# Kernel tuning notes

Measured on AMD Instinct MI355X. Metric: run time of the kernel, lower is better.

Reference implementation:

```python
import jax, jax.numpy as jnp
import numpy as np

N = 50000      # nodes
E = 800000     # edges (before self loops)
D_IN = 64      # input atom feature dim
HID = 128      # hidden_dim
HEADS = 4
C = HID // HEADS  # 32 per-head channels
ED = 12        # edge feature dim
L = 4          # num GAT layers
EPS = 1e-5


def setup_inputs() -> dict:
    key = jax.random.key(0)
    ks = jax.random.split(key, 10)
    s = 0.1
    return {
        "x": jax.random.normal(ks[0], (N, D_IN), jnp.float32),
        "edge_index": jax.random.randint(ks[1], (2, E), 0, N, dtype=jnp.int32),
        "edge_attr": jax.random.uniform(ks[2], (E, ED), jnp.float32),
        "Wp": jax.random.normal(ks[3], (D_IN, HID), jnp.float32) * s,
        "bp": jnp.zeros((HID,), jnp.float32),
        "W": jax.random.normal(ks[4], (L, HID, HID), jnp.float32) * s,
        "We": jax.random.normal(ks[5], (L, ED, HID), jnp.float32) * s,
        "att_src": jax.random.normal(ks[6], (L, HEADS, C), jnp.float32) * s,
        "att_dst": jax.random.normal(ks[7], (L, HEADS, C), jnp.float32) * s,
        "att_edge": jax.random.normal(ks[8], (L, HEADS, C), jnp.float32) * s,
        "bias": jnp.zeros((L, HID), jnp.float32),
        "gamma": jnp.ones((L, HID), jnp.float32),
        "beta": jnp.zeros((L, HID), jnp.float32),
    }


def _gat_layer(h, src, dst, ea_full, W, We, a_s, a_d, a_e, b):
    # PyG GATConv: x' = x W -> [N, heads, C]; attention uses edge features, msg = alpha * x'_src
    xp = (h @ W).reshape(N, HEADS, C)
    e_emb = (ea_full @ We).reshape(-1, HEADS, C)          # [E', heads, C]
    a_src = (xp * a_s).sum(-1)                            # [N, heads]
    a_dst = (xp * a_d).sum(-1)
    a = a_src[src] + a_dst[dst] + (e_emb * a_e).sum(-1)   # [E', heads]
    a = jax.nn.leaky_relu(a, 0.2)
    # segment softmax over destination node neighborhoods
    amax = jax.ops.segment_max(a, dst, num_segments=N)
    ex = jnp.exp(a - amax[dst])
    denom = jax.ops.segment_sum(ex, dst, num_segments=N)
    alpha = ex / denom[dst]                               # [E', heads]
    msg = alpha[:, :, None] * xp[src]                     # [E', heads, C]
    out = jax.ops.segment_sum(msg, dst, num_segments=N)   # [N, heads, C]
    return out.reshape(N, HID) + b


def reference(x, edge_index, edge_attr, Wp, bp, W, We, att_src, att_dst, att_edge, bias, gamma, beta):
    # PyG GATConv add_self_loops=True with fill_value='mean' for edge_attr
    loop = jnp.arange(N, dtype=edge_index.dtype)
    src = jnp.concatenate([edge_index[0], loop])
    dst = jnp.concatenate([edge_index[1], loop])
    ea_mean = edge_attr.mean(0)
    ea_full = jnp.concatenate([edge_attr, jnp.broadcast_to(ea_mean, (N, ED))], 0)

    h = jax.nn.relu(x @ Wp + bp)
    for i in range(L):
        h_in = h
        h = _gat_layer(h, src, dst, ea_full, W[i], We[i], att_src[i], att_dst[i], att_edge[i], bias[i])
        # BatchNorm1d (training-mode batch statistics)
        mu = h.mean(0)
        var = ((h - mu) ** 2).mean(0)
        h = gamma[i] * (h - mu) / jnp.sqrt(var + EPS) + beta[i]
        h = jax.nn.relu(h)
        if i > 0:
            h = h + h_in
    return h
```

## Files before the change

kernel.cpp:

```cpp
#include <hip/hip_runtime.h>

constexpr int N_NODES = 50000;
constexpr int N_EDGES = 800000;
constexpr int N_ETOT  = N_EDGES + N_NODES;
constexpr int HID     = 128;
constexpr int HEADS   = 4;
constexpr int ED      = 12;
constexpr int LAYERS  = 4;
constexpr float BN_EPS = 1e-5f;
constexpr int SCAN_BLK = (N_NODES + 255) / 256;

typedef __attribute__((ext_vector_type(8))) short short8;
typedef __attribute__((ext_vector_type(4))) float floatx4;

__device__ inline unsigned bf16pair(float a, float b) {
    unsigned ua = __float_as_uint(a), ub = __float_as_uint(b);
    ua = (ua + 0x7FFFu + ((ua >> 16) & 1u)) >> 16;
    ub = (ub + 0x7FFFu + ((ub >> 16) & 1u)) >> 16;
    return ua | (ub << 16);
}

__global__ void hist_kernel(const int* __restrict__ dst, int* __restrict__ hist) {
    int e = blockIdx.x * blockDim.x + threadIdx.x;
    if (e >= N_ETOT) return;
    int d = (e < N_EDGES) ? dst[e] : (e - N_EDGES);
    atomicAdd(&hist[d], 1);
}

__global__ void blocksum_kernel(const int* __restrict__ hist, int* __restrict__ bsum) {
    __shared__ int sd[256];
    int t = threadIdx.x;
    int n = blockIdx.x * 256 + t;
    sd[t] = (n < N_NODES) ? hist[n] : 0;
    __syncthreads();
#pragma unroll
    for (int off = 128; off; off >>= 1) {
        if (t < off) sd[t] += sd[t + off];
        __syncthreads();
    }
    if (t == 0) bsum[blockIdx.x] = sd[0];
}

__global__ void bscan_kernel(const int* __restrict__ bsum, int* __restrict__ boff,
                             int* __restrict__ rowp) {
    __shared__ int sd[256];
    int t = threadIdx.x;
    int v = (t < SCAN_BLK) ? bsum[t] : 0;
    sd[t] = v;
    __syncthreads();
#pragma unroll
    for (int off = 1; off < 256; off <<= 1) {
        int u = (t >= off) ? sd[t - off] : 0;
        __syncthreads();
        sd[t] += u;
        __syncthreads();
    }
    if (t < SCAN_BLK) boff[t] = sd[t] - v;
    if (t == 255) rowp[N_NODES] = sd[255];
}

__global__ void rowp_kernel(const int* __restrict__ hist, const int* __restrict__ boff,
                            int* __restrict__ rowp, int* __restrict__ cursor) {
    __shared__ int sd[256];
    int t = threadIdx.x;
    int n = blockIdx.x * 256 + t;
    int v = (n < N_NODES) ? hist[n] : 0;
    sd[t] = v;
    __syncthreads();
#pragma unroll
    for (int off = 1; off < 256; off <<= 1) {
        int u = (t >= off) ? sd[t - off] : 0;
        __syncthreads();
        sd[t] += u;
        __syncthreads();
    }
    if (n < N_NODES) {
        int excl = sd[t] - v + boff[blockIdx.x];
        rowp[n] = excl;
        cursor[n] = excl;
    }
}

__global__ void scatter_kernel(const int* __restrict__ src, const int* __restrict__ dst,
                               int* __restrict__ cursor, int2* __restrict__ csr) {
    int e = blockIdx.x * blockDim.x + threadIdx.x;
    if (e >= N_ETOT) return;
    int s, d;
    if (e < N_EDGES) { s = src[e]; d = dst[e]; }
    else             { s = d = e - N_EDGES; }
    int pos = atomicAdd(&cursor[d], 1);
    csr[pos] = make_int2(s, e);
}

__launch_bounds__(256)
__global__ void eamean_kernel(const float* __restrict__ ea, float* __restrict__ easum) {
    __shared__ float ls[12];
    int t = threadIdx.x;
    if (t < 12) ls[t] = 0.f;
    __syncthreads();
    float loc[12];
#pragma unroll
    for (int d = 0; d < 12; d++) loc[d] = 0.f;
    int stride = gridDim.x * 256;
    for (int e = blockIdx.x * 256 + t; e < N_EDGES; e += stride) {
        const float* er = ea + (size_t)e * ED;
#pragma unroll
        for (int d = 0; d < 12; d++) loc[d] += er[d];
    }
#pragma unroll
    for (int d = 0; d < 12; d++) atomicAdd(&ls[d], loc[d]);
    __syncthreads();
    if (t < 12) atomicAdd(&easum[t], ls[t]);
}

__global__ void prep_kernel(const float* __restrict__ easum, const float* __restrict__ We,
                            const float* __restrict__ att_edge, float* __restrict__ wea_all,
                            float* __restrict__ aloop) {
    __shared__ float em[12];
    __shared__ float weash[LAYERS * ED * HEADS];
    int t = threadIdx.x;
    if (t < 12) em[t] = easum[t] / (float)N_EDGES;
    if (t < LAYERS * ED * HEADS) {
        int l = t / (ED * HEADS);
        int r = t % (ED * HEADS);
        int d = r / HEADS;
        int h = r % HEADS;
        float sum = 0.f;
#pragma unroll
        for (int c = 0; c < 32; c++)
            sum += We[((size_t)(l * ED + d)) * HID + h * 32 + c] *
                   att_edge[(l * HEADS + h) * 32 + c];
        wea_all[t] = sum;
        weash[t] = sum;
    }
    __syncthreads();
    if (t < LAYERS * HEADS) {
        int l = t / HEADS, h = t % HEADS;
        float s = 0.f;
#pragma unroll
        for (int d = 0; d < 12; d++) s += em[d] * weash[l * ED * HEADS + d * HEADS + h];
        aloop[t] = s;
    }
}

__launch_bounds__(256)
__global__ void aedgep_kernel(const int2* __restrict__ csr, const float* __restrict__ ea,
                              const float* __restrict__ wea_all, const float* __restrict__ aloop,
                              uint2* __restrict__ aecsr) {
    __shared__ float wsh[LAYERS * ED * HEADS];
    __shared__ float lsh[LAYERS * HEADS];
    int t = threadIdx.x;
    if (t < LAYERS * ED * HEADS) wsh[t] = wea_all[t];
    if (t < LAYERS * HEADS) lsh[t] = aloop[t];
    __syncthreads();
    int i = blockIdx.x * 256 + t;
    if (i >= N_ETOT) return;
    int e = csr[i].y;
    float a[LAYERS][4];
    if (e < N_EDGES) {
        float er[12];
        const float* ep = ea + (size_t)e * ED;
#pragma unroll
        for (int d = 0; d < 12; d++) er[d] = ep[d];
#pragma unroll
        for (int l = 0; l < LAYERS; l++) {
#pragma unroll
            for (int h = 0; h < 4; h++) {
                float s = 0.f;
#pragma unroll
                for (int d = 0; d < 12; d++) s += er[d] * wsh[l * 48 + d * 4 + h];
                a[l][h] = s;
            }
        }
    } else {
#pragma unroll
        for (int l = 0; l < LAYERS; l++)
#pragma unroll
            for (int h = 0; h < 4; h++) a[l][h] = lsh[l * 4 + h];
    }
#pragma unroll
    for (int l = 0; l < LAYERS; l++)
        aecsr[(size_t)l * N_ETOT + i] =
            make_uint2(bf16pair(a[l][0], a[l][1]), bf16pair(a[l][2], a[l][3]));
}

__global__ void packW_kernel(const float* __restrict__ W, unsigned short* __restrict__ wb) {
    int idx = blockIdx.x * 256 + threadIdx.x;
    if (idx >= LAYERS * HID * HID) return;
    int l = idx >> 14;
    int k = (idx >> 7) & 127;
    int n = idx & 127;
    unsigned u = __float_as_uint(W[idx]);
    u = (u + 0x7FFFu + ((u >> 16) & 1u)) >> 16;
    int kt = k >> 5, q = (k & 31) >> 3, j = k & 7;
    int nt = n >> 4, c = n & 15;
    int lane = q * 16 + c;
    wb[(size_t)l * 16384 + ((size_t)(kt * 8 + nt) * 64 + lane) * 8 + j] = (unsigned short)u;
}

__launch_bounds__(256)
__global__ void gemm0_kernel(const float* __restrict__ A, const float* __restrict__ B,
                             const float* __restrict__ bias, float* __restrict__ C,
                             unsigned* __restrict__ Cb) {
    constexpr int K = 64;
    __shared__ float Bs[K * 128];
    int t = threadIdx.x;
    const float4* B4 = (const float4*)B;
    float4* Bs4 = (float4*)Bs;
#pragma unroll
    for (int i = t; i < K * 32; i += 256) Bs4[i] = B4[i];
    __syncthreads();

    int c0 = (t & 15) * 8;
    int r0 = (t >> 4) * 4;
    int rbase = blockIdx.x * 64 + r0;

    float acc[4][8];
#pragma unroll
    for (int j = 0; j < 4; j++)
#pragma unroll
        for (int c = 0; c < 8; c++) acc[j][c] = 0.f;

    const float4* A4 = (const float4*)A;
    int rg[4];
#pragma unroll
    for (int j = 0; j < 4; j++) rg[j] = min(rbase + j, N_NODES - 1);

    for (int kk = 0; kk < K; kk += 4) {
        float4 av[4];
#pragma unroll
        for (int j = 0; j < 4; j++) av[j] = A4[(size_t)rg[j] * (K / 4) + (kk >> 2)];
        float a_arr[4][4];
#pragma unroll
        for (int j = 0; j < 4; j++) {
            a_arr[j][0] = av[j].x; a_arr[j][1] = av[j].y;
            a_arr[j][2] = av[j].z; a_arr[j][3] = av[j].w;
        }
#pragma unroll
        for (int jj = 0; jj < 4; jj++) {
            float4 b0 = Bs4[(kk + jj) * 32 + (c0 >> 2)];
            float4 b1 = Bs4[(kk + jj) * 32 + (c0 >> 2) + 1];
#pragma unroll
            for (int j = 0; j < 4; j++) {
                float a = a_arr[j][jj];
                acc[j][0] += a * b0.x; acc[j][1] += a * b0.y;
                acc[j][2] += a * b0.z; acc[j][3] += a * b0.w;
                acc[j][4] += a * b1.x; acc[j][5] += a * b1.y;
                acc[j][6] += a * b1.z; acc[j][7] += a * b1.w;
            }
        }
    }

#pragma unroll
    for (int j = 0; j < 4; j++) {
        int r = rbase + j;
        if (r < N_NODES) {
            float o[8];
#pragma unroll
            for (int c = 0; c < 8; c++) o[c] = fmaxf(acc[j][c] + bias[c0 + c], 0.f);
            ((float4*)(C + (size_t)r * 128 + c0))[0] = make_float4(o[0], o[1], o[2], o[3]);
            ((float4*)(C + (size_t)r * 128 + c0 + 4))[0] = make_float4(o[4], o[5], o[6], o[7]);
            uint4 pk;
            pk.x = bf16pair(o[0], o[1]); pk.y = bf16pair(o[2], o[3]);
            pk.z = bf16pair(o[4], o[5]); pk.w = bf16pair(o[6], o[7]);
            ((uint4*)(Cb + (size_t)r * 64 + (c0 >> 1)))[0] = pk;
        }
    }
}

__launch_bounds__(256)
__global__ void gemm_mfma_kernel(const unsigned short* __restrict__ hAb,
                                 const unsigned short* __restrict__ wb,
                                 const float* __restrict__ att_s,
                                 const float* __restrict__ att_d,
                                 unsigned* __restrict__ xpb,
                                 float* __restrict__ asrc, float* __restrict__ adst) {
    __shared__ float lds[4][16][129];
    int t = threadIdx.x;
    int w = t >> 6, lane = t & 63;
    int rbase = blockIdx.x * 64 + w * 16;
    int mrow = lane & 15, quad = lane >> 4;

    floatx4 acc[8];
#pragma unroll
    for (int nt = 0; nt < 8; nt++) acc[nt] = (floatx4){0.f, 0.f, 0.f, 0.f};

    int arow = min(rbase + mrow, N_NODES - 1);
    const short8* wb8 = (const short8*)wb;
#pragma unroll
    for (int kt = 0; kt < 4; kt++) {
        short8 afrag = *(const short8*)(hAb + (size_t)arow * 128 + kt * 32 + quad * 8);
#pragma unroll
        for (int nt = 0; nt < 8; nt++) {
            short8 bfrag = wb8[(kt * 8 + nt) * 64 + lane];
            acc[nt] = __builtin_amdgcn_mfma_f32_16x16x32_bf16(afrag, bfrag, acc[nt], 0, 0, 0);
        }
    }

#pragma unroll
    for (int nt = 0; nt < 8; nt++)
#pragma unroll
        for (int rr = 0; rr < 4; rr++)
            lds[w][quad * 4 + rr][nt * 16 + mrow] = acc[nt][rr];

    int row = lane >> 2, h = lane & 3;
    int r = rbase + row;
    float vals[32];
    float ps = 0.f, pd = 0.f;
#pragma unroll
    for (int c = 0; c < 32; c++) {
        float v = lds[w][row][h * 32 + c];
        vals[c] = v;
        ps += v * att_s[h * 32 + c];
        pd += v * att_d[h * 32 + c];
    }
    if (r < N_NODES) {
        unsigned* dstp = xpb + (size_t)r * 64 + h * 16;
#pragma unroll
        for (int qq = 0; qq < 4; qq++) {
            uint4 o;
            o.x = bf16pair(vals[qq * 8 + 0], vals[qq * 8 + 1]);
            o.y = bf16pair(vals[qq * 8 + 2], vals[qq * 8 + 3]);
            o.z = bf16pair(vals[qq * 8 + 4], vals[qq * 8 + 5]);
            o.w = bf16pair(vals[qq * 8 + 6], vals[qq * 8 + 7]);
            ((uint4*)dstp)[qq] = o;
        }
        asrc[r * 4 + h] = ps;
        adst[r * 4 + h] = pd;
    }
}

__launch_bounds__(256)
__global__ void node_kernel(const uint2* __restrict__ aecsr, const float* __restrict__ asrc,
                            const float* __restrict__ adst, const int* __restrict__ rowp,
                            const int2* __restrict__ csr, const unsigned* __restrict__ xpb,
                            float* __restrict__ out) {
    int gw = (blockIdx.x * blockDim.x + threadIdx.x) >> 6;
    int lane = threadIdx.x & 63;
    if (gw >= N_NODES) return;
    int sub = lane >> 4;
    int sl  = lane & 15;
    int h   = sl >> 2;
    int beg = rowp[gw], end = rowp[gw + 1];
    const uint4* xp4 = (const uint4*)xpb;
    float adh = adst[gw * 4 + h];

    float a[8];
#pragma unroll
    for (int c = 0; c < 8; c++) a[c] = 0.f;
    float den = 0.f;

#define PROC(JJ)                                                                 \
    {                                                                            \
        int2 se = csr[JJ];                                                       \
        uint2 ae = aecsr[JJ];                                                    \
        unsigned aw = (h & 2) ? ae.y : ae.x;                                     \
        float aeh = __uint_as_float((h & 1) ? (aw & 0xFFFF0000u) : (aw << 16));  \
        float ash = asrc[se.x * 4 + h];                                          \
        uint4 v = xp4[(size_t)se.x * 16 + sl];                                   \
        float lg = ash + adh + aeh;                                              \
        lg = (lg > 0.f) ? lg : 0.2f * lg;                                        \
        float ex = __expf(fminf(lg, 60.f));                                      \
        a[0] += ex * __uint_as_float(v.x << 16);                                 \
        a[1] += ex * __uint_as_float(v.x & 0xFFFF0000u);                         \
        a[2] += ex * __uint_as_float(v.y << 16);                                 \
        a[3] += ex * __uint_as_float(v.y & 0xFFFF0000u);                         \
        a[4] += ex * __uint_as_float(v.z << 16);                                 \
        a[5] += ex * __uint_as_float(v.z & 0xFFFF0000u);                         \
        a[6] += ex * __uint_as_float(v.w << 16);                                 \
        a[7] += ex * __uint_as_float(v.w & 0xFFFF0000u);                         \
        den += ex;                                                               \
    }

    int j = beg + sub;
    for (; j + 12 < end; j += 16) {
        PROC(j); PROC(j + 4); PROC(j + 8); PROC(j + 12);
    }
    for (; j < end; j += 4) PROC(j);
#undef PROC

#pragma unroll
    for (int c = 0; c < 8; c++) {
        a[c] += __shfl_xor(a[c], 16);
        a[c] += __shfl_xor(a[c], 32);
    }
    den += __shfl_xor(den, 16);
    den += __shfl_xor(den, 32);
    float inv = 1.0f / den;
    if (sub == 0) {
        float* op = out + (size_t)gw * 128 + sl * 8;
        ((float4*)op)[0] = make_float4(a[0] * inv, a[1] * inv, a[2] * inv, a[3] * inv);
        ((float4*)op)[1] = make_float4(a[4] * inv, a[5] * inv, a[6] * inv, a[7] * inv);
    }
}

__launch_bounds__(256)
__global__ void bnstats_kernel(const float* __restrict__ h, float* __restrict__ bnsum,
                               float* __restrict__ bnsum2) {
    __shared__ float ls[256], ls2[256];
    int t = threadIdx.x;
    int c = t & 127, half = t >> 7;
    int r0 = blockIdx.x * 128;
    float s = 0.f, s2 = 0.f;
    int rend = min(r0 + 128, N_NODES);
    for (int r = r0 + half; r < rend; r += 2) {
        float v = h[(size_t)r * 128 + c];
        s += v; s2 += v * v;
    }
    ls[t] = s; ls2[t] = s2;
    __syncthreads();
    if (half == 0) {
        s += ls[t + 128]; s2 += ls2[t + 128];
        atomicAdd(&bnsum[c], s);
        atomicAdd(&bnsum2[c], s2);
    }
}

__launch_bounds__(256)
__global__ void update_kernel(const float* __restrict__ outb, const float* __restrict__ bnsum,
                              const float* __restrict__ bnsum2, const float* __restrict__ gamma,
                              const float* __restrict__ beta, const float* __restrict__ hA,
                              float* __restrict__ dst, unsigned* __restrict__ dstb,
                              int add_res) {
    __shared__ float sc_s[128], sh_s[128];
    int t = threadIdx.x;
    if (t < 128) {
        float mu = bnsum[t] / (float)N_NODES;
        float var = bnsum2[t] / (float)N_NODES - mu * mu;
        float inv = rsqrtf(var + BN_EPS);
        float g = gamma[t] * inv;
        sc_s[t] = g;
        sh_s[t] = beta[t] - mu * g;
    }
    __syncthreads();
    int i = blockIdx.x * blockDim.x + t;
    if (i >= N_NODES * 32) return;
    int c4 = (i & 31) * 4;
    float4 o = ((const float4*)outb)[i];
    float4 v;
    v.x = fmaxf(o.x * sc_s[c4 + 0] + sh_s[c4 + 0], 0.f);
    v.y = fmaxf(o.y * sc_s[c4 + 1] + sh_s[c4 + 1], 0.f);
    v.z = fmaxf(o.z * sc_s[c4 + 2] + sh_s[c4 + 2], 0.f);
    v.w = fmaxf(o.w * sc_s[c4 + 3] + sh_s[c4 + 3], 0.f);
    if (add_res) {
        float4 hh = ((const float4*)hA)[i];
        v.x += hh.x; v.y += hh.y; v.z += hh.z; v.w += hh.w;
    }
    ((float4*)dst)[i] = v;
    ((uint2*)dstb)[i] = make_uint2(bf16pair(v.x, v.y), bf16pair(v.z, v.w));
}

extern "C" void kernel_launch(void* const* d_in, const int* in_sizes, int n_in,
                              void* d_out, int out_size, void* d_ws, size_t ws_size,
                              hipStream_t stream) {
    const float* x          = (const float*)d_in[0];
    const int*   edge_index = (const int*)d_in[1];
    const float* edge_attr  = (const float*)d_in[2];
    const float* Wp         = (const float*)d_in[3];
    const float* bp         = (const float*)d_in[4];
    const float* W          = (const float*)d_in[5];
    const float* We         = (const float*)d_in[6];
    const float* att_src    = (const float*)d_in[7];
    const float* att_dst    = (const float*)d_in[8];
    const float* att_edge   = (const float*)d_in[9];
    const float* gamma      = (const float*)d_in[11];
    const float* beta       = (const float*)d_in[12];
    float* outp = (float*)d_out;

    const int* ei_src = edge_index;
    const int* ei_dst = edge_index + N_EDGES;

    char* p = (char*)d_ws;
    auto alloc = [&](size_t nbytes) {
        char* r = p;
        p += (nbytes + 255) & ~(size_t)255;
        return r;
    };
    int*   hist     = (int*)alloc((size_t)N_NODES * 4);
    float* easum    = (float*)alloc(16 * 4);
    float* bnsumall = (float*)alloc((size_t)LAYERS * 256 * 4);
    size_t zero_bytes = (char*)(bnsumall + LAYERS * 256) - (char*)hist;

    float* hA       = (float*)alloc((size_t)N_NODES * 128 * 4);
    unsigned* hAb   = (unsigned*)alloc((size_t)N_NODES * 64 * 4);
    unsigned* xpb   = (unsigned*)alloc((size_t)N_NODES * 64 * 4);
    float* outb     = (float*)alloc((size_t)N_NODES * 128 * 4);
    float* asrc     = (float*)alloc((size_t)N_NODES * 4 * 4);
    float* adst     = (float*)alloc((size_t)N_NODES * 4 * 4);
    float* wea_all  = (float*)alloc((LAYERS * 48 + 16) * 4);
    float* aloop    = wea_all + LAYERS * 48;
    unsigned short* wb = (unsigned short*)alloc((size_t)LAYERS * 16384 * 2);
    int* rowp       = (int*)alloc(((size_t)N_NODES + 1) * 4);
    int* cursor     = (int*)alloc((size_t)N_NODES * 4);
    int2* csr       = (int2*)alloc((size_t)N_ETOT * 8);
    uint2* aecsr    = (uint2*)alloc((size_t)LAYERS * N_ETOT * 8);
    int* bsum       = (int*)alloc(256 * 4);
    int* boff       = (int*)alloc(256 * 4);

    const int EB = (N_ETOT + 255) / 256;

    (void)hipMemsetAsync(hist, 0, zero_bytes, stream);

    hist_kernel<<<EB, 256, 0, stream>>>(ei_dst, hist);
    blocksum_kernel<<<SCAN_BLK, 256, 0, stream>>>(hist, bsum);
    bscan_kernel<<<1, 256, 0, stream>>>(bsum, boff, rowp);
    rowp_kernel<<<SCAN_BLK, 256, 0, stream>>>(hist, boff, rowp, cursor);
    scatter_kernel<<<EB, 256, 0, stream>>>(ei_src, ei_dst, cursor, csr);

    eamean_kernel<<<256, 256, 0, stream>>>(edge_attr, easum);
    prep_kernel<<<1, 256, 0, stream>>>(easum, We, att_edge, wea_all, aloop);
    packW_kernel<<<(LAYERS * HID * HID + 255) / 256, 256, 0, stream>>>(W, wb);
    aedgep_kernel<<<EB, 256, 0, stream>>>(csr, edge_attr, wea_all, aloop, aecsr);

    gemm0_kernel<<<(N_NODES + 63) / 64, 256, 0, stream>>>(x, Wp, bp, hA, hAb);

    for (int l = 0; l < LAYERS; l++) {
        float* bnsum  = bnsumall + l * 256;
        float* bnsum2 = bnsum + 128;
        gemm_mfma_kernel<<<(N_NODES + 63) / 64, 256, 0, stream>>>(
            (const unsigned short*)hAb, wb + (size_t)l * 16384,
            att_src + l * 128, att_dst + l * 128, xpb, asrc, adst);
        node_kernel<<<(N_NODES + 3) / 4, 256, 0, stream>>>(
            aecsr + (size_t)l * N_ETOT, asrc, adst, rowp, csr, xpb, outb);
        bnstats_kernel<<<(N_NODES + 127) / 128, 256, 0, stream>>>(outb, bnsum, bnsum2);
        float* dst = (l == LAYERS - 1) ? outp : hA;
        update_kernel<<<(N_NODES * 32 + 255) / 256, 256, 0, stream>>>(
            outb, bnsum, bnsum2, gamma + l * 128, beta + l * 128, hA, dst, hAb,
            (l > 0) ? 1 : 0);
    }
}
```

Before: 672.8 us.

## Merge independent preprocessing kernels and fuse BN update into next-layer GEMM

Independent setup kernels (histogram, edge-attr mean, weight packing, scatter, input GEMM, edge attention precompute, first-layer GEMM) are merged into combined launches that branch on block index, cutting launch count and letting unrelated work share one grid. The per-layer BatchNorm/ReLU/residual update is folded into the next layer's MFMA GEMM prologue, so it no longer writes a bf16 copy of h that is read back. A separate final update kernel handles the last layer. The merged kernels carry the union of shared-memory needs, which may lower occupancy for the lightweight branches.

New measurement: 638.4 us. 5.1% less time.

```diff
diff --git a/kernel.cpp b/kernel.cpp
--- a/kernel.cpp
+++ b/kernel.cpp
@@ -9,6 +9,9 @@
 constexpr int LAYERS  = 4;
 constexpr float BN_EPS = 1e-5f;
 constexpr int SCAN_BLK = (N_NODES + 255) / 256;
+constexpr int EB = (N_ETOT + 255) / 256;
+constexpr int GB = (N_NODES + 63) / 64;
+constexpr int WB = (LAYERS * HID * HID + 255) / 256;
 
 typedef __attribute__((ext_vector_type(8))) short short8;
 typedef __attribute__((ext_vector_type(4))) float floatx4;
@@ -20,11 +23,49 @@
     return ua | (ub << 16);
 }
 
-__global__ void hist_kernel(const int* __restrict__ dst, int* __restrict__ hist) {
-    int e = blockIdx.x * blockDim.x + threadIdx.x;
-    if (e >= N_ETOT) return;
-    int d = (e < N_EDGES) ? dst[e] : (e - N_EDGES);
-    atomicAdd(&hist[d], 1);
+__launch_bounds__(256)
+__global__ void pre1_kernel(const int* __restrict__ dst, int* __restrict__ hist,
+                            const float* __restrict__ ea, float* __restrict__ easum,
+                            const float* __restrict__ W, unsigned short* __restrict__ wb) {
+    __shared__ float ls[12];
+    int bid = blockIdx.x, t = threadIdx.x;
+    if (bid < EB) {
+        int e = bid * 256 + t;
+        if (e < N_ETOT) {
+            int d = (e < N_EDGES) ? dst[e] : (e - N_EDGES);
+            atomicAdd(&hist[d], 1);
+        }
+    } else if (bid < EB + 256) {
+        int b2 = bid - EB;
+        if (t < 12) ls[t] = 0.f;
+        __syncthreads();
+        float loc[12];
+#pragma unroll
+        for (int d = 0; d < 12; d++) loc[d] = 0.f;
+        for (int e = b2 * 256 + t; e < N_EDGES; e += 256 * 256) {
+            const float* er = ea + (size_t)e * ED;
+#pragma unroll
+            for (int d = 0; d < 12; d++) loc[d] += er[d];
+        }
+#pragma unroll
+        for (int d = 0; d < 12; d++) atomicAdd(&ls[d], loc[d]);
+        __syncthreads();
+        if (t < 12) atomicAdd(&easum[t], ls[t]);
+    } else {
+        int idx = (bid - EB - 256) * 256 + t;
+        if (idx < LAYERS * HID * HID) {
+            int l = idx >> 14;
+            int k = (idx >> 7) & 127;
+            int n = idx & 127;
+            unsigned u = __float_as_uint(W[idx]);
+            u = (u + 0x7FFFu + ((u >> 16) & 1u)) >> 16;
+            int kt = k >> 5, q = (k & 31) >> 3, j = k & 7;
+            int nt = n >> 4, c = n & 15;
+            int lane = q * 16 + c;
+            wb[(size_t)l * 16384 + ((size_t)(kt * 8 + nt) * 64 + lane) * 8 + j] =
+                (unsigned short)u;
+        }
+    }
 }
 
 __global__ void blocksum_kernel(const int* __restrict__ hist, int* __restrict__ bsum) {
@@ -41,22 +82,52 @@
     if (t == 0) bsum[blockIdx.x] = sd[0];
 }
 
-__global__ void bscan_kernel(const int* __restrict__ bsum, int* __restrict__ boff,
-                             int* __restrict__ rowp) {
-    __shared__ int sd[256];
-    int t = threadIdx.x;
-    int v = (t < SCAN_BLK) ? bsum[t] : 0;
-    sd[t] = v;
-    __syncthreads();
-#pragma unroll
-    for (int off = 1; off < 256; off <<= 1) {
-        int u = (t >= off) ? sd[t - off] : 0;
-        __syncthreads();
-        sd[t] += u;
-        __syncthreads();
-    }
-    if (t < SCAN_BLK) boff[t] = sd[t] - v;
-    if (t == 255) rowp[N_NODES] = sd[255];
+__launch_bounds__(256)
+__global__ void pre2_kernel(const int* __restrict__ bsum, int* __restrict__ boff,
+                            int* __restrict__ rowp, const float* __restrict__ easum,
+                            const float* __restrict__ We, const float* __restrict__ att_edge,
+                            float* __restrict__ wea_all, float* __restrict__ aloop) {
+    int t = threadIdx.x;
+    if (blockIdx.x == 0) {
+        __shared__ int sd[256];
+        int v = (t < SCAN_BLK) ? bsum[t] : 0;
+        sd[t] = v;
+        __syncthreads();
+#pragma unroll
+        for (int off = 1; off < 256; off <<= 1) {
+            int u = (t >= off) ? sd[t - off] : 0;
+            __syncthreads();
+            sd[t] += u;
+            __syncthreads();
+        }
+        if (t < SCAN_BLK) boff[t] = sd[t] - v;
+        if (t == 255) rowp[N_NODES] = sd[255];
+    } else {
+        __shared__ float em[12];
+        __shared__ float weash[LAYERS * ED * HEADS];
+        if (t < 12) em[t] = easum[t] / (float)N_EDGES;
+        if (t < LAYERS * ED * HEADS) {
+            int l = t / (ED * HEADS);
+            int r = t % (ED * HEADS);
+            int d = r / HEADS;
+            int h = r % HEADS;
+            float sum = 0.f;
+#pragma unroll
+            for (int c = 0; c < 32; c++)
+                sum += We[((size_t)(l * ED + d)) * HID + h * 32 + c] *
+                       att_edge[(l * HEADS + h) * 32 + c];
+            wea_all[t] = sum;
+            weash[t] = sum;
+        }
+        __syncthreads();
+        if (t < LAYERS * HEADS) {
+            int l = t / HEADS, h = t % HEADS;
+            float s = 0.f;
+#pragma unroll
+            for (int d = 0; d < 12; d++) s += em[d] * weash[l * ED * HEADS + d * HEADS + h];
+            aloop[t] = s;
+        }
+    }
 }
 
 __global__ void rowp_kernel(const int* __restrict__ hist, const int* __restrict__ boff,
@@ -81,130 +152,26 @@
     }
 }
 
-__global__ void scatter_kernel(const int* __restrict__ src, const int* __restrict__ dst,
-                               int* __restrict__ cursor, int2* __restrict__ csr) {
-    int e = blockIdx.x * blockDim.x + threadIdx.x;
-    if (e >= N_ETOT) return;
-    int s, d;
-    if (e < N_EDGES) { s = src[e]; d = dst[e]; }
-    else             { s = d = e - N_EDGES; }
-    int pos = atomicAdd(&cursor[d], 1);
-    csr[pos] = make_int2(s, e);
-}
-
-__launch_bounds__(256)
-__global__ void eamean_kernel(const float* __restrict__ ea, float* __restrict__ easum) {
-    __shared__ float ls[12];
-    int t = threadIdx.x;
-    if (t < 12) ls[t] = 0.f;
-    __syncthreads();
-    float loc[12];
-#pragma unroll
-    for (int d = 0; d < 12; d++) loc[d] = 0.f;
-    int stride = gridDim.x * 256;
-    for (int e = blockIdx.x * 256 + t; e < N_EDGES; e += stride) {
-        const float* er = ea + (size_t)e * ED;
-#pragma unroll
-        for (int d = 0; d < 12; d++) loc[d] += er[d];
-    }
-#pragma unroll
-    for (int d = 0; d < 12; d++) atomicAdd(&ls[d], loc[d]);
-    __syncthreads();
-    if (t < 12) atomicAdd(&easum[t], ls[t]);
-}
-
-__global__ void prep_kernel(const float* __restrict__ easum, const float* __restrict__ We,
-                            const float* __restrict__ att_edge, float* __restrict__ wea_all,
-                            float* __restrict__ aloop) {
-    __shared__ float em[12];
-    __shared__ float weash[LAYERS * ED * HEADS];
-    int t = threadIdx.x;
-    if (t < 12) em[t] = easum[t] / (float)N_EDGES;
-    if (t < LAYERS * ED * HEADS) {
-        int l = t / (ED * HEADS);
-        int r = t % (ED * HEADS);
-        int d = r / HEADS;
-        int h = r % HEADS;
-        float sum = 0.f;
-#pragma unroll
-        for (int c = 0; c < 32; c++)
-            sum += We[((size_t)(l * ED + d)) * HID + h * 32 + c] *
-                   att_edge[(l * HEADS + h) * 32 + c];
-        wea_all[t] = sum;
-        weash[t] = sum;
-    }
-    __syncthreads();
-    if (t < LAYERS * HEADS) {
-        int l = t / HEADS, h = t % HEADS;
-        float s = 0.f;
-#pragma unroll
-        for (int d = 0; d < 12; d++) s += em[d] * weash[l * ED * HEADS + d * HEADS + h];
-        aloop[t] = s;
-    }
-}
-
-__launch_bounds__(256)
-__global__ void aedgep_kernel(const int2* __restrict__ csr, const float* __restrict__ ea,
-                              const float* __restrict__ wea_all, const float* __restrict__ aloop,
-                              uint2* __restrict__ aecsr) {
-    __shared__ float wsh[LAYERS * ED * HEADS];
-    __shared__ float lsh[LAYERS * HEADS];
-    int t = threadIdx.x;
-    if (t < LAYERS * ED * HEADS) wsh[t] = wea_all[t];
-    if (t < LAYERS * HEADS) lsh[t] = aloop[t];
-    __syncthreads();
-    int i = blockIdx.x * 256 + t;
-    if (i >= N_ETOT) return;
-    int e = csr[i].y;
-    float a[LAYERS][4];
-    if (e < N_EDGES) {
-        float er[12];
-        const float* ep = ea + (size_t)e * ED;
-#pragma unroll
-        for (int d = 0; d < 12; d++) er[d] = ep[d];
-#pragma unroll
-        for (int l = 0; l < LAYERS; l++) {
-#pragma unroll
-            for (int h = 0; h < 4; h++) {
-                float s = 0.f;
-#pragma unroll
-                for (int d = 0; d < 12; d++) s += er[d] * wsh[l * 48 + d * 4 + h];
-                a[l][h] = s;
-            }
-        }
-    } else {
-#pragma unroll
-        for (int l = 0; l < LAYERS; l++)
-#pragma unroll
-            for (int h = 0; h < 4; h++) a[l][h] = lsh[l * 4 + h];
-    }
-#pragma unroll
-    for (int l = 0; l < LAYERS; l++)
-        aecsr[(size_t)l * N_ETOT + i] =
-            make_uint2(bf16pair(a[l][0], a[l][1]), bf16pair(a[l][2], a[l][3]));
-}
-
-__global__ void packW_kernel(const float* __restrict__ W, unsigned short* __restrict__ wb) {
-    int idx = blockIdx.x * 256 + threadIdx.x;
-    if (idx >= LAYERS * HID * HID) return;
-    int l = idx >> 14;
-    int k = (idx >> 7) & 127;
-    int n = idx & 127;
-    unsigned u = __float_as_uint(W[idx]);
-    u = (u + 0x7FFFu + ((u >> 16) & 1u)) >> 16;
-    int kt = k >> 5, q = (k & 31) >> 3, j = k & 7;
-    int nt = n >> 4, c = n & 15;
-    int lane = q * 16 + c;
-    wb[(size_t)l * 16384 + ((size_t)(kt * 8 + nt) * 64 + lane) * 8 + j] = (unsigned short)u;
-}
-
-__launch_bounds__(256)
-__global__ void gemm0_kernel(const float* __restrict__ A, const float* __restrict__ B,
-                             const float* __restrict__ bias, float* __restrict__ C,
-                             unsigned* __restrict__ Cb) {
+__launch_bounds__(256)
+__global__ void pre3_kernel(const int* __restrict__ src, const int* __restrict__ dst,
+                            int* __restrict__ cursor, int2* __restrict__ csr,
+                            const float* __restrict__ A, const float* __restrict__ B,
+                            const float* __restrict__ bias, float* __restrict__ C,
+                            unsigned* __restrict__ Cb) {
+    __shared__ float Bs[64 * 128];
+    int t = threadIdx.x;
+    if (blockIdx.x < EB) {
+        int e = blockIdx.x * 256 + t;
+        if (e >= N_ETOT) return;
+        int s, d;
+        if (e < N_EDGES) { s = src[e]; d = dst[e]; }
+        else             { s = d = e - N_EDGES; }
+        int pos = atomicAdd(&cursor[d], 1);
+        csr[pos] = make_int2(s, e);
+        return;
+    }
     constexpr int K = 64;
-    __shared__ float Bs[K * 128];
-    int t = threadIdx.x;
+    int bid = blockIdx.x - EB;
     const float4* B4 = (const float4*)B;
     float4* Bs4 = (float4*)Bs;
 #pragma unroll
@@ -213,7 +180,7 @@
 
     int c0 = (t & 15) * 8;
     int r0 = (t >> 4) * 4;
-    int rbase = blockIdx.x * 64 + r0;
+    int rbase = bid * 64 + r0;
 
     float acc[4][8];
 #pragma unroll
@@ -269,27 +236,173 @@
 }
 
 __launch_bounds__(256)
-__global__ void gemm_mfma_kernel(const unsigned short* __restrict__ hAb,
-                                 const unsigned short* __restrict__ wb,
-                                 const float* __restrict__ att_s,
-                                 const float* __restrict__ att_d,
-                                 unsigned* __restrict__ xpb,
-                                 float* __restrict__ asrc, float* __restrict__ adst) {
+__global__ void pre4_kernel(const int2* __restrict__ csr, const float* __restrict__ ea,
+                            const float* __restrict__ wea_all, const float* __restrict__ aloop,
+                            uint2* __restrict__ aecsr,
+                            const unsigned short* __restrict__ hAb,
+                            const unsigned short* __restrict__ wb,
+                            const float* __restrict__ att_s, const float* __restrict__ att_d,
+                            unsigned* __restrict__ xpb,
+                            float* __restrict__ asrc, float* __restrict__ adst) {
+    __shared__ float smem[4 * 16 * 129];
+    int t = threadIdx.x;
+    if (blockIdx.x < EB) {
+        float* wsh = smem;
+        float* lsh = smem + 192;
+        if (t < LAYERS * ED * HEADS) wsh[t] = wea_all[t];
+        if (t < LAYERS * HEADS) lsh[t] = aloop[t];
+        __syncthreads();
+        int i = blockIdx.x * 256 + t;
+        if (i >= N_ETOT) return;
+        int e = csr[i].y;
+        float a[LAYERS][4];
+        if (e < N_EDGES) {
+            float er[12];
+            const float* ep = ea + (size_t)e * ED;
+#pragma unroll
+            for (int d = 0; d < 12; d++) er[d] = ep[d];
+#pragma unroll
+            for (int l = 0; l < LAYERS; l++)
+#pragma unroll
+                for (int h = 0; h < 4; h++) {
+                    float s = 0.f;
+#pragma unroll
+                    for (int d = 0; d < 12; d++) s += er[d] * wsh[l * 48 + d * 4 + h];
+                    a[l][h] = s;
+                }
+        } else {
+#pragma unroll
+            for (int l = 0; l < LAYERS; l++)
+#pragma unroll
+                for (int h = 0; h < 4; h++) a[l][h] = lsh[l * 4 + h];
+        }
+#pragma unroll
+        for (int l = 0; l < LAYERS; l++)
+            aecsr[(size_t)l * N_ETOT + i] =
+                make_uint2(bf16pair(a[l][0], a[l][1]), bf16pair(a[l][2], a[l][3]));
+        return;
+    }
+    int bid = blockIdx.x - EB;
+    float (*lds)[16][129] = (float (*)[16][129])smem;
+    int w = t >> 6, lane = t & 63;
+    int rbase = bid * 64 + w * 16;
+    int mrow = lane & 15, quad = lane >> 4;
+
+    floatx4 acc[8];
+#pragma unroll
+    for (int nt = 0; nt < 8; nt++) acc[nt] = (floatx4){0.f, 0.f, 0.f, 0.f};
+
+    int arow = min(rbase + mrow, N_NODES - 1);
+    const short8* wb8 = (const short8*)wb;
+#pragma unroll
+    for (int kt = 0; kt < 4; kt++) {
+        short8 afrag = *(const short8*)(hAb + (size_t)arow * 128 + kt * 32 + quad * 8);
+#pragma unroll
+        for (int nt = 0; nt < 8; nt++) {
+            short8 bfrag = wb8[(kt * 8 + nt) * 64 + lane];
+            acc[nt] = __builtin_amdgcn_mfma_f32_16x16x32_bf16(afrag, bfrag, acc[nt], 0, 0, 0);
+        }
+    }
+#pragma unroll
+    for (int nt = 0; nt < 8; nt++)
+#pragma unroll
+        for (int rr = 0; rr < 4; rr++)
+            lds[w][quad * 4 + rr][nt * 16 + mrow] = acc[nt][rr];
+
+    int row = lane >> 2, h = lane & 3;
+    int r = rbase + row;
+    float vals[32];
+    float ps = 0.f, pd = 0.f;
+#pragma unroll
+    for (int c = 0; c < 32; c++) {
+        float v = lds[w][row][h * 32 + c];
+        vals[c] = v;
+        ps += v * att_s[h * 32 + c];
+        pd += v * att_d[h * 32 + c];
+    }
+    if (r < N_NODES) {
+        unsigned* dstp = xpb + (size_t)r * 64 + h * 16;
+#pragma unroll
+        for (int qq = 0; qq < 4; qq++) {
+            uint4 o;
+            o.x = bf16pair(vals[qq * 8 + 0], vals[qq * 8 + 1]);
+            o.y = bf16pair(vals[qq * 8 + 2], vals[qq * 8 + 3]);
+            o.z = bf16pair(vals[qq * 8 + 4], vals[qq * 8 + 5]);
+            o.w = bf16pair(vals[qq * 8 + 6], vals[qq * 8 + 7]);
+            ((uint4*)dstp)[qq] = o;
+        }
+        asrc[r * 4 + h] = ps;
+        adst[r * 4 + h] = pd;
+    }
+}
+
+template <int ADD>
+__launch_bounds__(256)
+__global__ void gemm_fused_kernel(const float* __restrict__ outb,
+                                  const float* __restrict__ bnsum,
+                                  const float* __restrict__ bnsum2,
+                                  const float* __restrict__ gamma,
+                                  const float* __restrict__ beta,
+                                  float* __restrict__ hA,
+                                  const unsigned short* __restrict__ wb,
+                                  const float* __restrict__ att_s,
+                                  const float* __restrict__ att_d,
+                                  unsigned* __restrict__ xpb,
+                                  float* __restrict__ asrc, float* __restrict__ adst) {
     __shared__ float lds[4][16][129];
-    int t = threadIdx.x;
+    __shared__ float sc_s[128], sh_s[128];
+    int t = threadIdx.x;
+    if (t < 128) {
+        float mu = bnsum[t] / (float)N_NODES;
+        float var = bnsum2[t] / (float)N_NODES - mu * mu;
+        float inv = rsqrtf(var + BN_EPS);
+        float g = gamma[t] * inv;
+        sc_s[t] = g;
+        sh_s[t] = beta[t] - mu * g;
+    }
+    __syncthreads();
+
     int w = t >> 6, lane = t & 63;
     int rbase = blockIdx.x * 64 + w * 16;
     int mrow = lane & 15, quad = lane >> 4;
+    int arow = rbase + mrow;
+    bool owner = arow < N_NODES;
+    int ar = min(arow, N_NODES - 1);
 
     floatx4 acc[8];
 #pragma unroll
     for (int nt = 0; nt < 8; nt++) acc[nt] = (floatx4){0.f, 0.f, 0.f, 0.f};
 
-    int arow = min(rbase + mrow, N_NODES - 1);
     const short8* wb8 = (const short8*)wb;
 #pragma unroll
     for (int kt = 0; kt < 4; kt++) {
-        short8 afrag = *(const short8*)(hAb + (size_t)arow * 128 + kt * 32 + quad * 8);
+        int cb = kt * 32 + quad * 8;
+        const float4* ob = (const float4*)(outb + (size_t)ar * 128 + cb);
+        float4 o0 = ob[0], o1 = ob[1];
+        float v[8];
+        v[0] = fmaxf(o0.x * sc_s[cb + 0] + sh_s[cb + 0], 0.f);
+        v[1] = fmaxf(o0.y * sc_s[cb + 1] + sh_s[cb + 1], 0.f);
+        v[2] = fmaxf(o0.z * sc_s[cb + 2] + sh_s[cb + 2], 0.f);
+        v[3] = fmaxf(o0.w * sc_s[cb + 3] + sh_s[cb + 3], 0.f);
+        v[4] = fmaxf(o1.x * sc_s[cb + 4] + sh_s[cb + 4], 0.f);
+        v[5] = fmaxf(o1.y * sc_s[cb + 5] + sh_s[cb + 5], 0.f);
+        v[6] = fmaxf(o1.z * sc_s[cb + 6] + sh_s[cb + 6], 0.f);
+        v[7] = fmaxf(o1.w * sc_s[cb + 7] + sh_s[cb + 7], 0.f);
+        if (ADD) {
+            const float4* hp = (const float4*)(hA + (size_t)ar * 128 + cb);
+            float4 h0 = hp[0], h1 = hp[1];
+            v[0] += h0.x; v[1] += h0.y; v[2] += h0.z; v[3] += h0.w;
+            v[4] += h1.x; v[5] += h1.y; v[6] += h1.z; v[7] += h1.w;
+        }
+        if (owner) {
+            float4* hw = (float4*)(hA + (size_t)ar * 128 + cb);
+            hw[0] = make_float4(v[0], v[1], v[2], v[3]);
+            hw[1] = make_float4(v[4], v[5], v[6], v[7]);
+        }
+        uint4 pk;
+        pk.x = bf16pair(v[0], v[1]); pk.y = bf16pair(v[2], v[3]);
+        pk.z = bf16pair(v[4], v[5]); pk.w = bf16pair(v[6], v[7]);
+        short8 afrag = *(short8*)&pk;
 #pragma unroll
         for (int nt = 0; nt < 8; nt++) {
             short8 bfrag = wb8[(kt * 8 + nt) * 64 + lane];
@@ -417,11 +530,10 @@
 }
 
 __launch_bounds__(256)
-__global__ void update_kernel(const float* __restrict__ outb, const float* __restrict__ bnsum,
-                              const float* __restrict__ bnsum2, const float* __restrict__ gamma,
-                              const float* __restrict__ beta, const float* __restrict__ hA,
-                              float* __restrict__ dst, unsigned* __restrict__ dstb,
-                              int add_res) {
+__global__ void finalupd_kernel(const float* __restrict__ outb, const float* __restrict__ bnsum,
+                                const float* __restrict__ bnsum2, const float* __restrict__ gamma,
+                                const float* __restrict__ beta, const float* __restrict__ hA,
+                                float* __restrict__ dst) {
     __shared__ float sc_s[128], sh_s[128];
     int t = threadIdx.x;
     if (t < 128) {
@@ -437,17 +549,13 @@
     if (i >= N_NODES * 32) return;
     int c4 = (i & 31) * 4;
     float4 o = ((const float4*)outb)[i];
+    float4 hh = ((const float4*)hA)[i];
     float4 v;
-    v.x = fmaxf(o.x * sc_s[c4 + 0] + sh_s[c4 + 0], 0.f);
-    v.y = fmaxf(o.y * sc_s[c4 + 1] + sh_s[c4 + 1], 0.f);
-    v.z = fmaxf(o.z * sc_s[c4 + 2] + sh_s[c4 + 2], 0.f);
-    v.w = fmaxf(o.w * sc_s[c4 + 3] + sh_s[c4 + 3], 0.f);
-    if (add_res) {
-        float4 hh = ((const float4*)hA)[i];
-        v.x += hh.x; v.y += hh.y; v.z += hh.z; v.w += hh.w;
-    }
+    v.x = fmaxf(o.x * sc_s[c4 + 0] + sh_s[c4 + 0], 0.f) + hh.x;
+    v.y = fmaxf(o.y * sc_s[c4 + 1] + sh_s[c4 + 1], 0.f) + hh.y;
+    v.z = fmaxf(o.z * sc_s[c4 + 2] + sh_s[c4 + 2], 0.f) + hh.z;
+    v.w = fmaxf(o.w * sc_s[c4 + 3] + sh_s[c4 + 3], 0.f) + hh.w;
     ((float4*)dst)[i] = v;
-    ((uint2*)dstb)[i] = make_uint2(bf16pair(v.x, v.y), bf16pair(v.z, v.w));
 }
 
 extern "C" void kernel_launch(void* const* d_in, const int* in_sizes, int n_in,
@@ -497,35 +605,37 @@
     int* bsum       = (int*)alloc(256 * 4);
     int* boff       = (int*)alloc(256 * 4);
 
-    const int EB = (N_ETOT + 255) / 256;
-
     (void)hipMemsetAsync(hist, 0, zero_bytes, stream);
 
-    hist_kernel<<<EB, 256, 0, stream>>>(ei_dst, hist);
+    pre1_kernel<<<EB + 256 + WB, 256, 0, stream>>>(ei_dst, hist, edge_attr, easum, W, wb);
     blocksum_kernel<<<SCAN_BLK, 256, 0, stream>>>(hist, bsum);
-    bscan_kernel<<<1, 256, 0, stream>>>(bsum, boff, rowp);
+    pre2_kernel<<<2, 256, 0, stream>>>(bsum, boff, rowp, easum, We, att_edge, wea_all, aloop);
     rowp_kernel<<<SCAN_BLK, 256, 0, stream>>>(hist, boff, rowp, cursor);
-    scatter_kernel<<<EB, 256, 0, stream>>>(ei_src, ei_dst, cursor, csr);
-
-    eamean_kernel<<<256, 256, 0, stream>>>(edge_attr, easum);
-    prep_kernel<<<1, 256, 0, stream>>>(easum, We, att_edge, wea_all, aloop);
-    packW_kernel<<<(LAYERS * HID * HID + 255) / 256, 256, 0, stream>>>(W, wb);
-    aedgep_kernel<<<EB, 256, 0, stream>>>(csr, edge_attr, wea_all, aloop, aecsr);
-
-    gemm0_kernel<<<(N_NODES + 63) / 64, 256, 0, stream>>>(x, Wp, bp, hA, hAb);
+    pre3_kernel<<<EB + GB, 256, 0, stream>>>(ei_src, ei_dst, cursor, csr, x, Wp, bp, hA, hAb);
+    pre4_kernel<<<EB + GB, 256, 0, stream>>>(csr, edge_attr, wea_all, aloop, aecsr,
+                                             (const unsigned short*)hAb, wb,
+                                             att_src, att_dst, xpb, asrc, adst);
 
     for (int l = 0; l < LAYERS; l++) {
         float* bnsum  = bnsumall + l * 256;
         float* bnsum2 = bnsum + 128;
-        gemm_mfma_kernel<<<(N_NODES + 63) / 64, 256, 0, stream>>>(
-            (const unsigned short*)hAb, wb + (size_t)l * 16384,
-            att_src + l * 128, att_dst + l * 128, xpb, asrc, adst);
         node_kernel<<<(N_NODES + 3) / 4, 256, 0, stream>>>(
             aecsr + (size_t)l * N_ETOT, asrc, adst, rowp, csr, xpb, outb);
         bnstats_kernel<<<(N_NODES + 127) / 128, 256, 0, stream>>>(outb, bnsum, bnsum2);
-        float* dst = (l == LAYERS - 1) ? outp : hA;
-        update_kernel<<<(N_NODES * 32 + 255) / 256, 256, 0, stream>>>(
-            outb, bnsum, bnsum2, gamma + l * 128, beta + l * 128, hA, dst, hAb,
-            (l > 0) ? 1 : 0);
-    }
-}
+        if (l < LAYERS - 1) {
+            if (l == 0)
+                gemm_fused_kernel<0><<<GB, 256, 0, stream>>>(
+                    outb, bnsum, bnsum2, gamma + l * 128, beta + l * 128, hA,
+                    wb + (size_t)(l + 1) * 16384, att_src + (l + 1) * 128,
+                    att_dst + (l + 1) * 128, xpb, asrc, adst);
+            else
+                gemm_fused_kernel<1><<<GB, 256, 0, stream>>>(
+                    outb, bnsum, bnsum2, gamma + l * 128, beta + l * 128, hA,
+                    wb + (size_t)(l + 1) * 16384, att_src + (l + 1) * 128,
+                    att_dst + (l + 1) * 128, xpb, asrc, adst);
+        } else {
+            finalupd_kernel<<<(N_NODES * 32 + 255) / 256, 256, 0, stream>>>(
+                outb, bnsum, bnsum2, gamma + l * 128, beta + l * 128, hA, outp);
+        }
+    }
+}
```
